# Kernel tuning notes

Hardware: AMD Instinct MI355X
Metric: run time of the kernel (lower is better)

Reference implementation:

```python
import jax, jax.numpy as jnp
import numpy as np

ATOMS_PER_RES = 24  # hard-coded in .view(B, N_l, -1, 24)
NEG_SLOPE = 0.01    # nn.LeakyReLU default


def setup_inputs() -> dict:
    key = jax.random.key(0)
    ks = jax.random.split(key, 10)
    B, N_l, N_p, H, G = 16, 64, 512, 128, 10
    pos_l = jax.random.normal(ks[0], (B, N_l, 3), jnp.float32) * 5.0
    pos_p = jax.random.normal(ks[1], (B, N_p, ATOMS_PER_RES, 3), jnp.float32) * 5.0
    Interact = jax.random.normal(ks[2], (B, N_l, N_p, H), jnp.float32)
    Interact_mask = jax.random.randint(ks[3], (B, N_l, N_p), 0, 2) > 0
    W_pi = jax.random.normal(ks[4], (H, G), jnp.float32) * 0.05
    b_pi = jnp.zeros((G,), jnp.float32)
    W_sigma = jax.random.normal(ks[5], (H, G), jnp.float32) * 0.05
    b_sigma = jnp.zeros((G,), jnp.float32)
    W_mu = jax.random.normal(ks[6], (H, G), jnp.float32) * 0.05
    b_mu = jnp.zeros((G,), jnp.float32)
    return {
        "pos_l": pos_l, "pos_p": pos_p, "Interact": Interact,
        "Interact_mask": Interact_mask,
        "W_pi": W_pi, "b_pi": b_pi,
        "W_sigma": W_sigma, "b_sigma": b_sigma,
        "W_mu": W_mu, "b_mu": b_mu,
    }


def _min_dist(pos_l, pos_p):
    # pos_l: [B, N_l, 3]; pos_p: [B, N_p, 24, 3]
    B, N_l, _ = pos_l.shape
    Y = pos_p.reshape(B, -1, 3)  # [B, N_p*24, 3]
    d2 = (jnp.sum(pos_l * pos_l, axis=-1)[..., None]
          + jnp.sum(Y * Y, axis=-1)[:, None, :]
          - 2.0 * jnp.einsum('bic,bjc->bij', pos_l, Y))  # [B, N_l, N_p*24]
    dist = jnp.nan_to_num(jnp.sqrt(d2), nan=10000.0)
    # min over the 24 atoms of each residue -> [B, N_l, N_p]
    return dist.reshape(B, N_l, -1, ATOMS_PER_RES).min(axis=-1)


def reference(pos_l, pos_p, Interact, Interact_mask,
              W_pi, b_pi, W_sigma, b_sigma, W_mu, b_mu):
    leaky = lambda x: jax.nn.leaky_relu(x, NEG_SLOPE)
    dist = _min_dist(pos_l, pos_p)                       # [B, N_l, N_p]
    # original gathers dist[Interact_mask]; keep static shape, zero-fill masked-out
    dist_masked = jnp.where(Interact_mask, dist, 0.0)
    pi = jax.nn.softmax(Interact @ W_pi + b_pi, axis=-1)          # [B,N_l,N_p,G]
    sigma = jnp.clip(leaky(Interact @ W_sigma + b_sigma) + 1.1, 1e-6, None)
    mu = leaky(Interact @ W_mu + b_mu) + 1.0
    return pi, sigma, mu, dist_masked, Interact_mask
```

## Files before the change

### kernel.cpp

```cpp
#include <hip/hip_runtime.h>
#include <cmath>

#define NB 16
#define NL 64
#define NP 512
#define NH 128
#define NG 10
#define ROWS (NB * NL * NP)

#define OFF_PI    ((size_t)0)
#define OFF_SIGMA ((size_t)5242880)
#define OFF_MU    ((size_t)10485760)
#define OFF_DIST  ((size_t)15728640)
#define OFF_MASK  ((size_t)16252928)

__global__ __launch_bounds__(256) void k_dist(
    const float* __restrict__ pos_l,
    const float* __restrict__ pos_p,
    const int*   __restrict__ mask,
    float* __restrict__ dist_out,
    float* __restrict__ mask_out)
{
    int idx = blockIdx.x * 256 + threadIdx.x;
    int p  = idx & (NP - 1);
    int bl = idx >> 9;
    int b  = bl >> 6;

    const float* xl = pos_l + bl * 3;
    float x0 = xl[0], x1 = xl[1], x2 = xl[2];
    float xs = x0 * x0 + x1 * x1 + x2 * x2;

    const float4* yp = (const float4*)(pos_p + ((size_t)(b * NP + p)) * 72);

    float m = 1e30f;
    #pragma unroll
    for (int q = 0; q < 6; ++q) {
        float4 v0 = yp[q * 3 + 0];
        float4 v1 = yp[q * 3 + 1];
        float4 v2 = yp[q * 3 + 2];
        float c[12] = {v0.x, v0.y, v0.z, v0.w,
                       v1.x, v1.y, v1.z, v1.w,
                       v2.x, v2.y, v2.z, v2.w};
        #pragma unroll
        for (int a = 0; a < 4; ++a) {
            float yx = c[a * 3 + 0], yy = c[a * 3 + 1], yz = c[a * 3 + 2];
            float d2 = xs + (yx * yx + yy * yy + yz * yz)
                          - 2.0f * (x0 * yx + x1 * yy + x2 * yz);
            float s = (d2 >= 0.0f) ? sqrtf(d2) : 10000.0f;
            m = fminf(m, s);
        }
    }

    int mk = mask[idx];
    dist_out[idx] = mk ? m : 0.0f;
    mask_out[idx] = mk ? 1.0f : 0.0f;
}

__global__ __launch_bounds__(256) void k_gemv(
    const float* __restrict__ X,
    const float* __restrict__ Wpi, const float* __restrict__ bpi,
    const float* __restrict__ Wsg, const float* __restrict__ bsg,
    const float* __restrict__ Wmu, const float* __restrict__ bmu,
    float* __restrict__ out_pi,
    float* __restrict__ out_sg,
    float* __restrict__ out_mu)
{
    __shared__ float lw[NH * 32];
    __shared__ float lb[32];
    int tid = threadIdx.x;

    for (int i = tid; i < NH * 32; i += 256) {
        int k = i >> 5, g = i & 31;
        float v = 0.0f;
        if      (g < 10) v = Wpi[k * NG + g];
        else if (g < 20) v = Wsg[k * NG + (g - 10)];
        else if (g < 30) v = Wmu[k * NG + (g - 20)];
        lw[i] = v;
    }
    if (tid < 32) {
        float v = 0.0f;
        if      (tid < 10) v = bpi[tid];
        else if (tid < 20) v = bsg[tid - 10];
        else if (tid < 30) v = bmu[tid - 20];
        lb[tid] = v;
    }
    __syncthreads();

    int row = blockIdx.x * 256 + tid;
    const float4* xr  = (const float4*)(X + (size_t)row * NH);
    const float4* lw4 = (const float4*)lw;

    float4 acc[8];
    #pragma unroll
    for (int g4 = 0; g4 < 8; ++g4) acc[g4] = ((const float4*)lb)[g4];

    #pragma unroll 4
    for (int k4 = 0; k4 < 32; ++k4) {
        float4 h = xr[k4];
        float hk[4] = {h.x, h.y, h.z, h.w};
        #pragma unroll
        for (int kk = 0; kk < 4; ++kk) {
            const float4* wrow = lw4 + (size_t)(k4 * 4 + kk) * 8;
            float hv = hk[kk];
            #pragma unroll
            for (int g4 = 0; g4 < 8; ++g4) {
                float4 w = wrow[g4];
                acc[g4].x = fmaf(hv, w.x, acc[g4].x);
                acc[g4].y = fmaf(hv, w.y, acc[g4].y);
                acc[g4].z = fmaf(hv, w.z, acc[g4].z);
                acc[g4].w = fmaf(hv, w.w, acc[g4].w);
            }
        }
    }

    float a[32];
    #pragma unroll
    for (int g4 = 0; g4 < 8; ++g4) {
        a[g4 * 4 + 0] = acc[g4].x; a[g4 * 4 + 1] = acc[g4].y;
        a[g4 * 4 + 2] = acc[g4].z; a[g4 * 4 + 3] = acc[g4].w;
    }

    size_t ro = (size_t)row * NG;

    float mx = a[0];
    #pragma unroll
    for (int g = 1; g < NG; ++g) mx = fmaxf(mx, a[g]);
    float e[NG], s = 0.0f;
    #pragma unroll
    for (int g = 0; g < NG; ++g) { e[g] = __expf(a[g] - mx); s += e[g]; }
    float inv = 1.0f / s;
    #pragma unroll
    for (int g = 0; g < NG; ++g) out_pi[ro + g] = e[g] * inv;

    #pragma unroll
    for (int g = 0; g < NG; ++g) {
        float x = a[10 + g];
        float v = (x >= 0.0f ? x : 0.01f * x) + 1.1f;
        out_sg[ro + g] = fmaxf(v, 1e-6f);
    }

    #pragma unroll
    for (int g = 0; g < NG; ++g) {
        float x = a[20 + g];
        out_mu[ro + g] = (x >= 0.0f ? x : 0.01f * x) + 1.0f;
    }
}

extern "C" void kernel_launch(void* const* d_in, const int* in_sizes, int n_in,
                              void* d_out, int out_size, void* d_ws, size_t ws_size,
                              hipStream_t stream) {
    const float* pos_l    = (const float*)d_in[0];
    const float* pos_p    = (const float*)d_in[1];
    const float* Interact = (const float*)d_in[2];
    const int*   mask     = (const int*)  d_in[3];
    const float* Wpi      = (const float*)d_in[4];
    const float* bpi      = (const float*)d_in[5];
    const float* Wsg      = (const float*)d_in[6];
    const float* bsg      = (const float*)d_in[7];
    const float* Wmu      = (const float*)d_in[8];
    const float* bmu      = (const float*)d_in[9];

    float* out      = (float*)d_out;
    float* out_pi   = out + OFF_PI;
    float* out_sg   = out + OFF_SIGMA;
    float* out_mu   = out + OFF_MU;
    float* out_dist = out + OFF_DIST;
    float* out_mask = out + OFF_MASK;

    hipLaunchKernelGGL(k_dist, dim3(ROWS / 256), dim3(256), 0, stream,
                       pos_l, pos_p, mask, out_dist, out_mask);
    hipLaunchKernelGGL(k_gemv, dim3(ROWS / 256), dim3(256), 0, stream,
                       Interact, Wpi, bpi, Wsg, bsg, Wmu, bmu,
                       out_pi, out_sg, out_mu);
}
```

Before: 450.2 us.

## Fuse distance and GEMV kernels with LDS-staged coalesced Interact loads

```diff
diff --git a/kernel.cpp b/kernel.cpp
--- a/kernel.cpp
+++ b/kernel.cpp
@@ -14,134 +14,123 @@
 #define OFF_DIST  ((size_t)15728640)
 #define OFF_MASK  ((size_t)16252928)
 
-__global__ __launch_bounds__(256) void k_dist(
+__global__ __launch_bounds__(256, 4) void k_fused(
     const float* __restrict__ pos_l,
     const float* __restrict__ pos_p,
     const int*   __restrict__ mask,
-    float* __restrict__ dist_out,
-    float* __restrict__ mask_out)
-{
-    int idx = blockIdx.x * 256 + threadIdx.x;
-    int p  = idx & (NP - 1);
-    int bl = idx >> 9;
-    int b  = bl >> 6;
-
-    const float* xl = pos_l + bl * 3;
-    float x0 = xl[0], x1 = xl[1], x2 = xl[2];
-    float xs = x0 * x0 + x1 * x1 + x2 * x2;
-
-    const float4* yp = (const float4*)(pos_p + ((size_t)(b * NP + p)) * 72);
-
-    float m = 1e30f;
-    #pragma unroll
-    for (int q = 0; q < 6; ++q) {
-        float4 v0 = yp[q * 3 + 0];
-        float4 v1 = yp[q * 3 + 1];
-        float4 v2 = yp[q * 3 + 2];
-        float c[12] = {v0.x, v0.y, v0.z, v0.w,
-                       v1.x, v1.y, v1.z, v1.w,
-                       v2.x, v2.y, v2.z, v2.w};
-        #pragma unroll
-        for (int a = 0; a < 4; ++a) {
-            float yx = c[a * 3 + 0], yy = c[a * 3 + 1], yz = c[a * 3 + 2];
-            float d2 = xs + (yx * yx + yy * yy + yz * yz)
-                          - 2.0f * (x0 * yx + x1 * yy + x2 * yz);
-            float s = (d2 >= 0.0f) ? sqrtf(d2) : 10000.0f;
-            m = fminf(m, s);
-        }
-    }
-
-    int mk = mask[idx];
-    dist_out[idx] = mk ? m : 0.0f;
-    mask_out[idx] = mk ? 1.0f : 0.0f;
-}
-
-__global__ __launch_bounds__(256) void k_gemv(
     const float* __restrict__ X,
     const float* __restrict__ Wpi, const float* __restrict__ bpi,
     const float* __restrict__ Wsg, const float* __restrict__ bsg,
     const float* __restrict__ Wmu, const float* __restrict__ bmu,
     float* __restrict__ out_pi,
     float* __restrict__ out_sg,
-    float* __restrict__ out_mu)
+    float* __restrict__ out_mu,
+    float* __restrict__ dist_out,
+    float* __restrict__ mask_out)
 {
-    __shared__ float lw[NH * 32];
-    __shared__ float lb[32];
-    int tid = threadIdx.x;
+    __shared__ float xs[256 * 33];
 
-    for (int i = tid; i < NH * 32; i += 256) {
-        int k = i >> 5, g = i & 31;
-        float v = 0.0f;
-        if      (g < 10) v = Wpi[k * NG + g];
-        else if (g < 20) v = Wsg[k * NG + (g - 10)];
-        else if (g < 30) v = Wmu[k * NG + (g - 20)];
-        lw[i] = v;
+    const int tid = threadIdx.x;
+    const int idx = blockIdx.x * 256 + tid;
+
+    {
+        int p  = idx & (NP - 1);
+        int bl = idx >> 9;
+        int b  = bl >> 6;
+
+        const float* xl = pos_l + bl * 3;
+        float x0 = xl[0], x1 = xl[1], x2 = xl[2];
+        float qs = x0 * x0 + x1 * x1 + x2 * x2;
+
+        const float4* yp = (const float4*)(pos_p + ((size_t)(b * NP + p)) * 72);
+
+        float m2 = 1e30f;
+        #pragma unroll
+        for (int q = 0; q < 6; ++q) {
+            float4 v0 = yp[q * 3 + 0];
+            float4 v1 = yp[q * 3 + 1];
+            float4 v2 = yp[q * 3 + 2];
+            float c[12] = {v0.x, v0.y, v0.z, v0.w,
+                           v1.x, v1.y, v1.z, v1.w,
+                           v2.x, v2.y, v2.z, v2.w};
+            #pragma unroll
+            for (int a = 0; a < 4; ++a) {
+                float yx = c[a * 3 + 0], yy = c[a * 3 + 1], yz = c[a * 3 + 2];
+                float d2 = qs + (yx * yx + yy * yy + yz * yz)
+                              - 2.0f * (x0 * yx + x1 * yy + x2 * yz);
+                d2 = (d2 >= 0.0f) ? d2 : 1e8f;
+                m2 = fminf(m2, d2);
+            }
+        }
+        float m = sqrtf(m2);
+
+        int mk = mask[idx];
+        dist_out[idx] = mk ? m : 0.0f;
+        mask_out[idx] = mk ? 1.0f : 0.0f;
     }
-    if (tid < 32) {
-        float v = 0.0f;
-        if      (tid < 10) v = bpi[tid];
-        else if (tid < 20) v = bsg[tid - 10];
-        else if (tid < 30) v = bmu[tid - 20];
-        lb[tid] = v;
+
+    float accp[NG], accs[NG], accm[NG];
+    #pragma unroll
+    for (int g = 0; g < NG; ++g) {
+        accp[g] = bpi[g];
+        accs[g] = bsg[g];
+        accm[g] = bmu[g];
     }
-    __syncthreads();
 
-    int row = blockIdx.x * 256 + tid;
-    const float4* xr  = (const float4*)(X + (size_t)row * NH);
-    const float4* lw4 = (const float4*)lw;
+    const size_t row0 = (size_t)blockIdx.x * 256;
 
-    float4 acc[8];
-    #pragma unroll
-    for (int g4 = 0; g4 < 8; ++g4) acc[g4] = ((const float4*)lb)[g4];
+    for (int kc = 0; kc < 4; ++kc) {
+        __syncthreads();
+        #pragma unroll
+        for (int j = 0; j < 8; ++j) {
+            int s  = j * 256 + tid;
+            int r  = s >> 3;
+            int k4 = s & 7;
+            float4 v = *(const float4*)(X + (row0 + r) * NH + kc * 32 + k4 * 4);
+            float* d = &xs[r * 33 + k4 * 4];
+            d[0] = v.x; d[1] = v.y; d[2] = v.z; d[3] = v.w;
+        }
+        __syncthreads();
 
-    #pragma unroll 4
-    for (int k4 = 0; k4 < 32; ++k4) {
-        float4 h = xr[k4];
-        float hk[4] = {h.x, h.y, h.z, h.w};
-        #pragma unroll
-        for (int kk = 0; kk < 4; ++kk) {
-            const float4* wrow = lw4 + (size_t)(k4 * 4 + kk) * 8;
-            float hv = hk[kk];
+        const float* xr = &xs[tid * 33];
+        #pragma unroll 4
+        for (int k = 0; k < 32; ++k) {
+            float h = xr[k];
+            int kk = kc * 32 + k;
+            const float* wp = Wpi + kk * NG;
+            const float* ws = Wsg + kk * NG;
+            const float* wm = Wmu + kk * NG;
             #pragma unroll
-            for (int g4 = 0; g4 < 8; ++g4) {
-                float4 w = wrow[g4];
-                acc[g4].x = fmaf(hv, w.x, acc[g4].x);
-                acc[g4].y = fmaf(hv, w.y, acc[g4].y);
-                acc[g4].z = fmaf(hv, w.z, acc[g4].z);
-                acc[g4].w = fmaf(hv, w.w, acc[g4].w);
+            for (int g = 0; g < NG; ++g) {
+                accp[g] = fmaf(h, wp[g], accp[g]);
+                accs[g] = fmaf(h, ws[g], accs[g]);
+                accm[g] = fmaf(h, wm[g], accm[g]);
             }
         }
     }
 
-    float a[32];
+    size_t ro = (size_t)idx * NG;
+
+    float mx = accp[0];
     #pragma unroll
-    for (int g4 = 0; g4 < 8; ++g4) {
-        a[g4 * 4 + 0] = acc[g4].x; a[g4 * 4 + 1] = acc[g4].y;
-        a[g4 * 4 + 2] = acc[g4].z; a[g4 * 4 + 3] = acc[g4].w;
-    }
-
-    size_t ro = (size_t)row * NG;
-
-    float mx = a[0];
+    for (int g = 1; g < NG; ++g) mx = fmaxf(mx, accp[g]);
+    float e[NG], ssum = 0.0f;
     #pragma unroll
-    for (int g = 1; g < NG; ++g) mx = fmaxf(mx, a[g]);
-    float e[NG], s = 0.0f;
-    #pragma unroll
-    for (int g = 0; g < NG; ++g) { e[g] = __expf(a[g] - mx); s += e[g]; }
-    float inv = 1.0f / s;
+    for (int g = 0; g < NG; ++g) { e[g] = __expf(accp[g] - mx); ssum += e[g]; }
+    float inv = 1.0f / ssum;
     #pragma unroll
     for (int g = 0; g < NG; ++g) out_pi[ro + g] = e[g] * inv;
 
     #pragma unroll
     for (int g = 0; g < NG; ++g) {
-        float x = a[10 + g];
+        float x = accs[g];
         float v = (x >= 0.0f ? x : 0.01f * x) + 1.1f;
         out_sg[ro + g] = fmaxf(v, 1e-6f);
     }
 
     #pragma unroll
     for (int g = 0; g < NG; ++g) {
-        float x = a[20 + g];
+        float x = accm[g];
         out_mu[ro + g] = (x >= 0.0f ? x : 0.01f * x) + 1.0f;
     }
 }
@@ -167,9 +156,8 @@
     float* out_dist = out + OFF_DIST;
     float* out_mask = out + OFF_MASK;
 
-    hipLaunchKernelGGL(k_dist, dim3(ROWS / 256), dim3(256), 0, stream,
-                       pos_l, pos_p, mask, out_dist, out_mask);
-    hipLaunchKernelGGL(k_gemv, dim3(ROWS / 256), dim3(256), 0, stream,
-                       Interact, Wpi, bpi, Wsg, bsg, Wmu, bmu,
-                       out_pi, out_sg, out_mu);
+    hipLaunchKernelGGL(k_fused, dim3(ROWS / 256), dim3(256), 0, stream,
+                       pos_l, pos_p, mask, Interact,
+                       Wpi, bpi, Wsg, bsg, Wmu, bmu,
+                       out_pi, out_sg, out_mu, out_dist, out_mask);
 }
```

After: 427.4 us. 1.05x faster.
